# Kernel tuning notes

Measured on AMD Instinct MI355X. Metric: run time of the kernel, lower is better.

The kernel has to match this reference:

```python
import jax, jax.numpy as jnp
import numpy as np

DIM = 2048
HEAD = 256
SEQ = 4096

def setup_inputs() -> dict:
    key = jax.random.key(0)
    ks = jax.random.split(key, 7)
    s = 1.0 / np.sqrt(DIM)
    return {
        "marketStateBatch": jax.random.normal(ks[0], (SEQ, DIM), dtype=jnp.float32),
        "Wq": jax.random.uniform(ks[1], (HEAD, DIM), jnp.float32, -s, s),
        "bq": jax.random.uniform(ks[2], (HEAD,), jnp.float32, -s, s),
        "Wk": jax.random.uniform(ks[3], (HEAD, DIM), jnp.float32, -s, s),
        "bk": jax.random.uniform(ks[4], (HEAD,), jnp.float32, -s, s),
        "Wv": jax.random.uniform(ks[5], (HEAD, DIM), jnp.float32, -s, s),
        "bv": jax.random.uniform(ks[6], (HEAD,), jnp.float32, -s, s),
    }

def reference(marketStateBatch, Wq, bq, Wk, bk, Wv, bv):
    x = marketStateBatch  # [S, D]
    q = x @ Wq.T + bq     # [S, H]
    k = x @ Wk.T + bk     # [S, H]
    v = x @ Wv.T + bv     # [S, H]
    # NOTE: original scales by sqrt(dimensionSize), the INPUT dim, not head dim.
    scores = (q @ k.T) * (1.0 / np.sqrt(DIM))  # [S, S]
    S = x.shape[0]
    causal = jnp.tril(jnp.ones((S, S), dtype=bool))
    scores = jnp.where(causal, scores, -jnp.inf)
    attn = jax.nn.softmax(scores, axis=-1)
    # torch.nan_to_num(attn, 0.0): rows are never all -inf here (diag kept),
    # but replicate the op faithfully.
    attn = jnp.nan_to_num(attn, nan=0.0)
    return attn @ v  # [S, H]
```

## Files before the change

### kernel.cpp

```cpp
#include <hip/hip_runtime.h>
#include <stdint.h>

#define SEQ 4096
#define DIMK 2048
#define HD 256

typedef __attribute__((ext_vector_type(8))) short bf16x8;
typedef __attribute__((ext_vector_type(4))) short u16x4;
typedef __attribute__((ext_vector_type(4))) float f32x4;
typedef __attribute__((ext_vector_type(16))) float f32x16;
typedef unsigned short u16;
typedef unsigned int u32;

#define BAR() asm volatile("s_barrier" ::: "memory")
#define VMCNT(n) asm volatile("s_waitcnt vmcnt(" #n ")" ::: "memory")

__device__ __forceinline__ u16 f2bf(float f) {
    u32 u = __float_as_uint(f);
    u += 0x7FFFu + ((u >> 16) & 1u);
    return (u16)(u >> 16);
}

__device__ __forceinline__ float bf2f(u16 h) {
    u32 u = ((u32)h) << 16;
    return __uint_as_float(u);
}

__device__ __forceinline__ bf16x8 pack8(f32x4 a0, f32x4 a1) {
    bf16x8 v8;
    v8[0]=(short)f2bf(a0[0]); v8[1]=(short)f2bf(a0[1]);
    v8[2]=(short)f2bf(a0[2]); v8[3]=(short)f2bf(a0[3]);
    v8[4]=(short)f2bf(a1[0]); v8[5]=(short)f2bf(a1[1]);
    v8[6]=(short)f2bf(a1[2]); v8[7]=(short)f2bf(a1[3]);
    return v8;
}

__device__ __forceinline__ void gl16(const void* g, void* l) {
    __builtin_amdgcn_global_load_lds(
        (const __attribute__((address_space(1))) void*)g,
        (__attribute__((address_space(3))) void*)l, 16, 0, 0);
}

__device__ __forceinline__ u32 cvtpk(float lo, float hi) {
    u32 d;
    asm("v_cvt_pk_bf16_f32 %0, %1, %2" : "=v"(d) : "v"(lo), "v"(hi));
    return d;
}

__device__ __forceinline__ void plswap(u32& x, u32& y) {
#if __has_builtin(__builtin_amdgcn_permlane32_swap)
    typedef int i32x2 __attribute__((ext_vector_type(2)));
    i32x2 r = __builtin_amdgcn_permlane32_swap((int)x, (int)y, false, false);
    x = (u32)r[0]; y = (u32)r[1];
#else
    asm("v_permlane32_swap_b32 %0, %1" : "+v"(x), "+v"(y));
#endif
}

__global__ __launch_bounds__(256) void cvt_all2(
    const float* __restrict__ x, const float* __restrict__ Wq,
    const float* __restrict__ Wk, const float* __restrict__ Wv,
    u16* __restrict__ xb_sw, u16* __restrict__ wb_sw)
{
    const int y = blockIdx.y;
    int i = blockIdx.x * 256 + threadIdx.x;
    int stride = gridDim.x * 256;
    if (y == 0) {
        for (; i < SEQ*DIMK/8; i += stride) {
            int row = i >> 8, c8 = i & 255;
            f32x4 a0 = *(const f32x4*)(x + (size_t)row*DIMK + c8*8);
            f32x4 a1 = *(const f32x4*)(x + (size_t)row*DIMK + c8*8 + 4);
            int mt = row >> 6, rl = row & 63, kt = c8 >> 3, sl = c8 & 7;
            size_t dst = ((size_t)(mt*32 + kt))*4096 + rl*64 + ((sl ^ (rl&7))*8);
            *(bf16x8*)(xb_sw + dst) = pack8(a0, a1);
        }
    } else {
        const float* W = (y==1) ? Wq : (y==2) ? Wk : Wv;
        for (; i < HD*DIMK/8; i += stride) {
            int row = i >> 8, c8 = i & 255;
            f32x4 a0 = *(const f32x4*)(W + (size_t)row*DIMK + c8*8);
            f32x4 a1 = *(const f32x4*)(W + (size_t)row*DIMK + c8*8 + 4);
            int gr = (y-1)*256 + row;
            int nt = gr >> 7, rl = gr & 127, kt = c8 >> 3, sl = c8 & 7;
            size_t dst = ((size_t)(nt*32 + kt))*8192 + rl*64 + ((sl ^ (rl&7))*8);
            *(bf16x8*)(wb_sw + dst) = pack8(a0, a1);
        }
    }
}

__global__ __launch_bounds__(256) void qkv_gemm2(
    const u16* __restrict__ xb_sw, const u16* __restrict__ wb_sw,
    const float* __restrict__ bq, const float* __restrict__ bk,
    const float* __restrict__ bv,
    u16* __restrict__ qb, u16* __restrict__ kb_t, u16* __restrict__ vt_t)
{
    __shared__ char T[2][24576];

    const int tid = threadIdx.x;
    const int lane = tid & 63;
    const int w = tid >> 6;
    const int r = lane & 15, g = lane >> 4;
    const int wr = w >> 1, wc = w & 1;
    const int mt = blockIdx.x;
    const int y  = blockIdx.y;
    const int z  = y >> 1;
    const float* bias = (z==0) ? bq : (z==1) ? bk : bv;

    const u16* abase = xb_sw + (size_t)mt*32*4096;
    const u16* bbase = wb_sw + (size_t)y*32*8192;

    f32x4 zero = {0.f,0.f,0.f,0.f};
    f32x4 acc[2][4];
    #pragma unroll
    for (int m = 0; m < 2; ++m)
        #pragma unroll
        for (int n = 0; n < 4; ++n) acc[m][n] = zero;

    auto stage = [&](int b, int kt) {
        const u16* ag = abase + (size_t)kt*4096 + w*1024 + lane*8;
        const u16* bg = bbase + (size_t)kt*8192 + w*2048 + lane*8;
        char* al = T[b] + w*2048;
        char* bl = T[b] + 8192 + w*4096;
        gl16(ag,        al);
        gl16(ag + 512,  al + 1024);
        gl16(bg,        bl);
        gl16(bg + 512,  bl + 1024);
        gl16(bg + 1024, bl + 2048);
        gl16(bg + 1536, bl + 3072);
    };

    stage(0, 0);
    stage(1, 1);

    for (int kt = 0; kt < 32; ++kt) {
        if (kt < 31) { VMCNT(6); } else { VMCNT(0); }
        BAR();
        const char* A = T[kt & 1];
        const char* B = T[kt & 1] + 8192;
        #pragma unroll
        for (int kc = 0; kc < 2; ++kc) {
            bf16x8 af[2], bfr[4];
            #pragma unroll
            for (int m = 0; m < 2; ++m) {
                int arow = wr*32 + m*16 + r;
                af[m] = *(const bf16x8*)(A + arow*128 + (((kc*4+g) ^ (arow&7)) << 4));
            }
            #pragma unroll
            for (int n = 0; n < 4; ++n) {
                int brow = wc*64 + n*16 + r;
                bfr[n] = *(const bf16x8*)(B + brow*128 + (((kc*4+g) ^ (brow&7)) << 4));
            }
            #pragma unroll
            for (int m = 0; m < 2; ++m)
                #pragma unroll
                for (int n = 0; n < 4; ++n)
                    acc[m][n] = __builtin_amdgcn_mfma_f32_16x16x32_bf16(
                        af[m], bfr[n], acc[m][n], 0, 0, 0);
        }
        BAR();
        if (kt + 2 < 32) stage(kt & 1, kt + 2);
    }

    const int m0 = mt*64, n0 = y*128;
    const float qs = 0.03187936f;
    if (z == 0) {
        #pragma unroll
        for (int n = 0; n < 4; ++n) {
            int hc = (n0 + wc*64 + n*16 + r) & 255;
            float bcol = bias[hc];
            #pragma unroll
            for (int m = 0; m < 2; ++m) {
                int row0 = m0 + wr*32 + m*16 + g*4;
                #pragma unroll
                for (int j = 0; j < 4; ++j)
                    qb[(size_t)(row0+j)*HD + hc] = f2bf((acc[m][n][j] + bcol) * qs);
            }
        }
    } else if (z == 1) {
        #pragma unroll
        for (int n = 0; n < 4; ++n) {
            int hc = (n0 + wc*64 + n*16 + r) & 255;
            float bcol = bias[hc];
            #pragma unroll
            for (int m = 0; m < 2; ++m) {
                int row0 = m0 + wr*32 + m*16 + g*4;
                #pragma unroll
                for (int j = 0; j < 4; ++j) {
                    int rowj = row0 + j;
                    int t = rowj >> 5, rl = rowj & 31;
                    kb_t[(size_t)t*8192 + rl*256 + (((hc>>3) ^ (rl&7))*8) + (hc&7)]
                        = f2bf(acc[m][n][j] + bcol);
                }
            }
        }
    } else {
        #pragma unroll
        for (int n = 0; n < 4; ++n) {
            int hc = (n0 + wc*64 + n*16 + r) & 255;
            float bcol = bias[hc];
            #pragma unroll
            for (int m = 0; m < 2; ++m) {
                int kv0 = m0 + wr*32 + m*16 + g*4;
                int t = kv0 >> 5, kl = kv0 & 31;
                u16x4 pk;
                #pragma unroll
                for (int j = 0; j < 4; ++j) pk[j] = (short)f2bf(acc[m][n][j] + bcol);
                *(u16x4*)(vt_t + (size_t)t*8192 + hc*32 +
                          (((kl>>3) ^ (hc&3) ^ ((hc>>2)&3))*8) + (kl&7)) = pk;
            }
        }
    }
}

__global__ __launch_bounds__(256, 2) void attn_part6(
    const u16* __restrict__ qb, const u16* __restrict__ kb_t,
    const u16* __restrict__ vt_t,
    u16* __restrict__ po, float* __restrict__ pm, float* __restrict__ pl,
    int C)
{
    __shared__ char Kb[2][16384];
    __shared__ char Vb[2][16384];

    const int pid = blockIdx.x;
    int Q = 0, a0 = 0;
    for (int k = 0; k < 32; ++k) {
        int nsk = (4*k + 4 + C - 1) / C;
        if (pid < a0 + nsk) { Q = k; break; }
        a0 += nsk;
    }
    const int s  = pid - a0;
    const int nt = 4*Q + 4;
    const int t0 = s*C;
    const int t1 = min(t0 + C, nt);

    const int tid = threadIdx.x;
    const int L = tid & 63;
    const int w = tid >> 6;
    const int l31 = L & 31;
    const int h   = L >> 5;
    const int qg  = Q*128 + w*32 + l31;
    const int vsw = (l31 & 3) ^ ((l31 >> 2) & 3);
    const int kx  = l31 & 7;

    auto stage = [&](int t, int b) {
        const u16* kg = kb_t + (size_t)t*8192 + w*2048 + L*8;
        const u16* vg = vt_t + (size_t)t*8192 + w*2048 + L*8;
        char* kl = Kb[b] + w*4096;
        char* vl = Vb[b] + w*4096;
        #pragma unroll
        for (int i = 0; i < 4; ++i) gl16(kg + i*512, kl + i*1024);
        #pragma unroll
        for (int i = 0; i < 4; ++i) gl16(vg + i*512, vl + i*1024);
    };

    stage(t0, t0 & 1);
    if (t0 + 1 < t1) stage(t0 + 1, (t0 + 1) & 1);
    else             stage(t0,     (t0 + 1) & 1);

    bf16x8 qf[16];
    {
        const u16* qp = qb + (size_t)qg*HD + h*8;
        #pragma unroll
        for (int c = 0; c < 16; ++c) qf[c] = *(const bf16x8*)(qp + c*16);
    }

    f32x16 o[8];
    #pragma unroll
    for (int ht = 0; ht < 8; ++ht)
        #pragma unroll
        for (int e = 0; e < 16; ++e) o[ht][e] = 0.f;
    float mrun = -1e30f, lrun = 0.f;

    for (int t = t0; t < t1; ++t) {
        if (t + 1 < t1) { VMCNT(8); } else { VMCNT(0); }
        BAR();
        const char* K = Kb[t & 1];
        const char* V = Vb[t & 1];

        #define LDK(c) (*(const bf16x8*)(K + l31*512 + (((2*(c) + h) ^ kx) << 4)))
        f32x16 sv;
        #pragma unroll
        for (int e = 0; e < 16; ++e) sv[e] = 0.f;
        __builtin_amdgcn_s_setprio(1);
        {
            bf16x8 ka = LDK(0), kb_ = LDK(1), kc = LDK(2), kd = LDK(3);
            sv = __builtin_amdgcn_mfma_f32_32x32x16_bf16(ka,  qf[0],  sv, 0,0,0); ka  = LDK(4);
            sv = __builtin_amdgcn_mfma_f32_32x32x16_bf16(kb_, qf[1],  sv, 0,0,0); kb_ = LDK(5);
            sv = __builtin_amdgcn_mfma_f32_32x32x16_bf16(kc,  qf[2],  sv, 0,0,0); kc  = LDK(6);
            sv = __builtin_amdgcn_mfma_f32_32x32x16_bf16(kd,  qf[3],  sv, 0,0,0); kd  = LDK(7);
            sv = __builtin_amdgcn_mfma_f32_32x32x16_bf16(ka,  qf[4],  sv, 0,0,0); ka  = LDK(8);
            sv = __builtin_amdgcn_mfma_f32_32x32x16_bf16(kb_, qf[5],  sv, 0,0,0); kb_ = LDK(9);
            sv = __builtin_amdgcn_mfma_f32_32x32x16_bf16(kc,  qf[6],  sv, 0,0,0); kc  = LDK(10);
            sv = __builtin_amdgcn_mfma_f32_32x32x16_bf16(kd,  qf[7],  sv, 0,0,0); kd  = LDK(11);
            sv = __builtin_amdgcn_mfma_f32_32x32x16_bf16(ka,  qf[8],  sv, 0,0,0); ka  = LDK(12);
            sv = __builtin_amdgcn_mfma_f32_32x32x16_bf16(kb_, qf[9],  sv, 0,0,0); kb_ = LDK(13);
            sv = __builtin_amdgcn_mfma_f32_32x32x16_bf16(kc,  qf[10], sv, 0,0,0); kc  = LDK(14);
            sv = __builtin_amdgcn_mfma_f32_32x32x16_bf16(kd,  qf[11], sv, 0,0,0); kd  = LDK(15);
            sv = __builtin_amdgcn_mfma_f32_32x32x16_bf16(ka,  qf[12], sv, 0,0,0);
            sv = __builtin_amdgcn_mfma_f32_32x32x16_bf16(kb_, qf[13], sv, 0,0,0);
            sv = __builtin_amdgcn_mfma_f32_32x32x16_bf16(kc,  qf[14], sv, 0,0,0);
            sv = __builtin_amdgcn_mfma_f32_32x32x16_bf16(kd,  qf[15], sv, 0,0,0);
        }
        #undef LDK
        __builtin_amdgcn_s_setprio(0);

        if (t*32 + 31 > Q*128 + w*32) {
            #pragma unroll
            for (int e = 0; e < 16; ++e) {
                int kvr = (e & 3) + 8*(e >> 2) + 4*h;
                if (t*32 + kvr > qg) sv[e] = -__builtin_inff();
            }
        }

        float m0_ = fmaxf(fmaxf(sv[0],sv[1]),  fmaxf(sv[2],sv[3]));
        float m1_ = fmaxf(fmaxf(sv[4],sv[5]),  fmaxf(sv[6],sv[7]));
        float m2_ = fmaxf(fmaxf(sv[8],sv[9]),  fmaxf(sv[10],sv[11]));
        float m3_ = fmaxf(fmaxf(sv[12],sv[13]),fmaxf(sv[14],sv[15]));
        float mx = fmaxf(fmaxf(m0_,m1_), fmaxf(m2_,m3_));
        mx = fmaxf(mx, __shfl_xor(mx, 32));
        if (__any(mx > mrun + 8.0f)) {
            float mnew  = fmaxf(mrun, mx);
            float alpha = exp2f(mrun - mnew);
            lrun *= alpha;
            #pragma unroll
            for (int ht = 0; ht < 8; ++ht) o[ht] *= alpha;
            mrun = mnew;
        }
        #pragma unroll
        for (int e = 0; e < 16; ++e) sv[e] = exp2f(sv[e] - mrun);
        float r0 = ((sv[0]+sv[1])+(sv[2]+sv[3])) + ((sv[4]+sv[5])+(sv[6]+sv[7]));
        float r1 = ((sv[8]+sv[9])+(sv[10]+sv[11])) + ((sv[12]+sv[13])+(sv[14]+sv[15]));
        float rs = r0 + r1;
        rs += __shfl_xor(rs, 32);
        lrun += rs;

        union { u32 wd[4]; bf16x8 v8; } up0, up1;
        {
            u32 A = cvtpk(sv[0],  sv[1]),  B = cvtpk(sv[2],  sv[3]);
            u32 Cc= cvtpk(sv[4],  sv[5]),  D = cvtpk(sv[6],  sv[7]);
            plswap(A, Cc); plswap(B, D);
            up0.wd[0]=A; up0.wd[1]=B; up0.wd[2]=Cc; up0.wd[3]=D;
            u32 A1 = cvtpk(sv[8],  sv[9]),  B1 = cvtpk(sv[10], sv[11]);
            u32 C1 = cvtpk(sv[12], sv[13]), D1 = cvtpk(sv[14], sv[15]);
            plswap(A1, C1); plswap(B1, D1);
            up1.wd[0]=A1; up1.wd[1]=B1; up1.wd[2]=C1; up1.wd[3]=D1;
        }
        bf16x8 pa0 = up0.v8, pa1 = up1.v8;

        __builtin_amdgcn_s_setprio(1);
        #pragma unroll
        for (int ht = 0; ht < 8; ++ht) {
            const char* vrow = V + (ht*32 + l31)*64;
            bf16x8 vf0 = *(const bf16x8*)(vrow + (((h)     ^ vsw) << 4));
            bf16x8 vf1 = *(const bf16x8*)(vrow + (((2 + h) ^ vsw) << 4));
            o[ht] = __builtin_amdgcn_mfma_f32_32x32x16_bf16(vf0, pa0, o[ht], 0, 0, 0);
            o[ht] = __builtin_amdgcn_mfma_f32_32x32x16_bf16(vf1, pa1, o[ht], 0, 0, 0);
        }
        __builtin_amdgcn_s_setprio(0);

        BAR();
        stage(min(t + 2, t1 - 1), t & 1);
    }

    VMCNT(0);

    if (h == 0) {
        pm[(size_t)pid*128 + w*32 + l31] = mrun;
        pl[(size_t)pid*128 + w*32 + l31] = lrun;
    }
    u16* op = po + ((size_t)pid*128 + w*32 + l31) * 256;
    #pragma unroll
    for (int ht = 0; ht < 8; ++ht)
        #pragma unroll
        for (int j = 0; j < 8; ++j) {
            u32 pk = (u32)f2bf(o[ht][2*j]) | ((u32)f2bf(o[ht][2*j+1]) << 16);
            int hdb = ht*32 + (j & 1)*2 + (j >> 1)*8 + 4*h;
            *(u32*)(op + hdb) = pk;
        }
}

__global__ __launch_bounds__(256) void attn_combine5(
    const u16* __restrict__ po, const float* __restrict__ pm,
    const float* __restrict__ pl, float* __restrict__ out, int C)
{
    const int tid = threadIdx.x;
    const int row = blockIdx.x * 16 + (tid >> 4);
    const int cg  = tid & 15;
    const int Q   = row >> 7, rr = row & 127;
    const int nt  = 4*Q + 4;
    const int ns  = (nt + C - 1) / C;
    int pid0 = 0;
    for (int k = 0; k < Q; ++k) pid0 += (4*k + 4 + C - 1) / C;

    float M = -1e30f;
    for (int s = 0; s < ns; ++s)
        M = fmaxf(M, pm[(size_t)(pid0+s)*128 + rr]);

    float lt = 0.f;
    f32x4 acc[4];
    f32x4 zero = {0.f,0.f,0.f,0.f};
    #pragma unroll
    for (int v = 0; v < 4; ++v) acc[v] = zero;

    for (int s = 0; s < ns; ++s) {
        float ms  = pm[(size_t)(pid0+s)*128 + rr];
        float wgt = exp2f(ms - M);
        lt += wgt * pl[(size_t)(pid0+s)*128 + rr];
        const u16* p = po + ((size_t)(pid0+s)*128 + rr)*256 + cg*16;
        #pragma unroll
        for (int v = 0; v < 4; ++v) {
            u16x4 pv = *(const u16x4*)(p + v*4);
            #pragma unroll
            for (int e = 0; e < 4; ++e)
                acc[v][e] += wgt * bf2f((u16)pv[e]);
        }
    }
    float inv = 1.f / lt;
    f32x4* op = (f32x4*)(out + (size_t)row*256 + cg*16);
    #pragma unroll
    for (int v = 0; v < 4; ++v) op[v] = acc[v] * inv;
}

extern "C" void kernel_launch(void* const* d_in, const int* in_sizes, int n_in,
                              void* d_out, int out_size, void* d_ws, size_t ws_size,
                              hipStream_t stream) {
    const float* x  = (const float*)d_in[0];
    const float* Wq = (const float*)d_in[1];
    const float* bq = (const float*)d_in[2];
    const float* Wk = (const float*)d_in[3];
    const float* bk = (const float*)d_in[4];
    const float* Wv = (const float*)d_in[5];
    const float* bv = (const float*)d_in[6];
    float* out = (float*)d_out;

    const size_t xb_bytes  = (size_t)SEQ * DIMK * 2;
    const size_t wb_bytes  = (size_t)768 * DIMK * 2;
    const size_t qkv_bytes = (size_t)SEQ * HD * 2;
    const size_t base = xb_bytes + wb_bytes + 3*qkv_bytes;

    int C = 64;
    size_t npid = 0;
    const int cand[4] = {5, 8, 16, 64};
    for (int ci = 0; ci < 4; ++ci) {
        int c = cand[ci];
        size_t np = 0;
        for (int k = 0; k < 32; ++k) np += (size_t)(4*k + 4 + c - 1) / c;
        size_t need = base + np * ((size_t)128*256*2 + 2*128*4);
        if (need <= ws_size) { C = c; npid = np; break; }
        if (ci == 3) { C = c; npid = np; }
    }

    char* p = (char*)d_ws;
    u16* xb_sw = (u16*)p; p += xb_bytes;
    u16* wb_sw = (u16*)p; p += wb_bytes;
    u16* qbuf  = (u16*)p; p += qkv_bytes;
    u16* kb_t  = (u16*)p; p += qkv_bytes;
    u16* vt_t  = (u16*)p; p += qkv_bytes;
    u16* po    = (u16*)p; p += npid * 128 * 256 * 2;
    float* pm  = (float*)p; p += npid * 128 * 4;
    float* pl  = (float*)p; p += npid * 128 * 4;

    cvt_all2<<<dim3(512, 4), 256, 0, stream>>>(x, Wq, Wk, Wv, xb_sw, wb_sw);

    qkv_gemm2<<<dim3(SEQ/64, 6), 256, 0, stream>>>(
        xb_sw, wb_sw, bq, bk, bv, qbuf, kb_t, vt_t);

    attn_part6<<<(int)npid, 256, 0, stream>>>(
        qbuf, kb_t, vt_t, po, pm, pl, C);

    attn_combine5<<<SEQ/16, 256, 0, stream>>>(po, pm, pl, out, C);
}
```

Measured before the change: 79.17 us.

## Enlarge QKV GEMM tile to 128x128 using 32x32x16 MFMA

The QKV projection GEMM goes from 64x128 block tiles to 128x128, so each block stages twice as many A rows and the grid halves. Each wave now computes a 64x64 sub-tile with 32x32x16 bf16 MFMAs instead of 16x16x32, which means fewer LDS fragment loads per FLOP. The change also raises wave priority around the MFMA section and sets a two-blocks-per-CU launch bound. The costs are more LDS per block, more accumulator registers, and only 192 blocks in the grid, which may leave some CUs idle.

```diff
diff --git a/kernel.cpp b/kernel.cpp
--- a/kernel.cpp
+++ b/kernel.cpp
@@ -88,125 +88,118 @@
     }
 }
 
-__global__ __launch_bounds__(256) void qkv_gemm2(
+__global__ __launch_bounds__(256, 2) void qkv_gemm3(
     const u16* __restrict__ xb_sw, const u16* __restrict__ wb_sw,
     const float* __restrict__ bq, const float* __restrict__ bk,
     const float* __restrict__ bv,
     u16* __restrict__ qb, u16* __restrict__ kb_t, u16* __restrict__ vt_t)
 {
-    __shared__ char T[2][24576];
+    __shared__ char Ab[2][16384];
+    __shared__ char Bb[2][16384];
 
     const int tid = threadIdx.x;
-    const int lane = tid & 63;
+    const int L = tid & 63;
     const int w = tid >> 6;
-    const int r = lane & 15, g = lane >> 4;
+    const int l31 = L & 31, h = L >> 5;
     const int wr = w >> 1, wc = w & 1;
-    const int mt = blockIdx.x;
-    const int y  = blockIdx.y;
-    const int z  = y >> 1;
+    const int mt2 = blockIdx.x;
+    const int y   = blockIdx.y;
+    const int z   = y >> 1;
     const float* bias = (z==0) ? bq : (z==1) ? bk : bv;
 
-    const u16* abase = xb_sw + (size_t)mt*32*4096;
-    const u16* bbase = wb_sw + (size_t)y*32*8192;
-
-    f32x4 zero = {0.f,0.f,0.f,0.f};
-    f32x4 acc[2][4];
-    #pragma unroll
-    for (int m = 0; m < 2; ++m)
-        #pragma unroll
-        for (int n = 0; n < 4; ++n) acc[m][n] = zero;
-
-    auto stage = [&](int b, int kt) {
-        const u16* ag = abase + (size_t)kt*4096 + w*1024 + lane*8;
-        const u16* bg = bbase + (size_t)kt*8192 + w*2048 + lane*8;
-        char* al = T[b] + w*2048;
-        char* bl = T[b] + 8192 + w*4096;
-        gl16(ag,        al);
-        gl16(ag + 512,  al + 1024);
-        gl16(bg,        bl);
-        gl16(bg + 512,  bl + 1024);
-        gl16(bg + 1024, bl + 2048);
-        gl16(bg + 1536, bl + 3072);
+    const u16* a0 = xb_sw + ((size_t)((mt2*2 + (w>>1))*32))*4096 + (w&1)*2048 + L*8;
+    const u16* b0 = wb_sw + ((size_t)(y*32))*8192 + w*2048 + L*8;
+
+    auto stage = [&](int kt, int b) {
+        const u16* ag = a0 + (size_t)kt*4096;
+        const u16* bg = b0 + (size_t)kt*8192;
+        char* al = Ab[b] + w*4096;
+        char* bl = Bb[b] + w*4096;
+        #pragma unroll
+        for (int i = 0; i < 4; ++i) gl16(ag + i*512, al + i*1024);
+        #pragma unroll
+        for (int i = 0; i < 4; ++i) gl16(bg + i*512, bl + i*1024);
     };
 
     stage(0, 0);
     stage(1, 1);
 
+    f32x16 acc[2][2];
+    #pragma unroll
+    for (int m = 0; m < 2; ++m)
+        #pragma unroll
+        for (int n = 0; n < 2; ++n)
+            #pragma unroll
+            for (int e = 0; e < 16; ++e) acc[m][n][e] = 0.f;
+
     for (int kt = 0; kt < 32; ++kt) {
-        if (kt < 31) { VMCNT(6); } else { VMCNT(0); }
+        if (kt < 31) { VMCNT(8); } else { VMCNT(0); }
         BAR();
-        const char* A = T[kt & 1];
-        const char* B = T[kt & 1] + 8192;
-        #pragma unroll
-        for (int kc = 0; kc < 2; ++kc) {
-            bf16x8 af[2], bfr[4];
+        const char* A = Ab[kt & 1];
+        const char* B = Bb[kt & 1];
+        __builtin_amdgcn_s_setprio(1);
+        #pragma unroll
+        for (int c = 0; c < 4; ++c) {
+            const int sl = 2*c + h;
+            bf16x8 af[2], bfr[2];
             #pragma unroll
             for (int m = 0; m < 2; ++m) {
-                int arow = wr*32 + m*16 + r;
-                af[m] = *(const bf16x8*)(A + arow*128 + (((kc*4+g) ^ (arow&7)) << 4));
+                int row = wr*64 + m*32 + l31;
+                af[m] = *(const bf16x8*)(A + (row>>6)*8192 + (row&63)*128
+                                           + ((sl ^ (row&7)) << 4));
             }
             #pragma unroll
-            for (int n = 0; n < 4; ++n) {
-                int brow = wc*64 + n*16 + r;
-                bfr[n] = *(const bf16x8*)(B + brow*128 + (((kc*4+g) ^ (brow&7)) << 4));
+            for (int n = 0; n < 2; ++n) {
+                int brow = wc*64 + n*32 + l31;
+                bfr[n] = *(const bf16x8*)(B + brow*128 + ((sl ^ (brow&7)) << 4));
             }
             #pragma unroll
             for (int m = 0; m < 2; ++m)
                 #pragma unroll
-                for (int n = 0; n < 4; ++n)
-                    acc[m][n] = __builtin_amdgcn_mfma_f32_16x16x32_bf16(
+                for (int n = 0; n < 2; ++n)
+                    acc[m][n] = __builtin_amdgcn_mfma_f32_32x32x16_bf16(
                         af[m], bfr[n], acc[m][n], 0, 0, 0);
         }
+        __builtin_amdgcn_s_setprio(0);
         BAR();
-        if (kt + 2 < 32) stage(kt & 1, kt + 2);
-    }
-
-    const int m0 = mt*64, n0 = y*128;
+        if (kt + 2 < 32) stage(kt + 2, kt & 1);
+    }
+
+    const int m0 = mt2*128;
     const float qs = 0.03187936f;
-    if (z == 0) {
-        #pragma unroll
-        for (int n = 0; n < 4; ++n) {
-            int hc = (n0 + wc*64 + n*16 + r) & 255;
-            float bcol = bias[hc];
-            #pragma unroll
-            for (int m = 0; m < 2; ++m) {
-                int row0 = m0 + wr*32 + m*16 + g*4;
+    #pragma unroll
+    for (int n = 0; n < 2; ++n) {
+        const int hc = ((y&1)*128 + wc*64 + n*32 + l31) & 255;
+        const float bcol = bias[hc];
+        #pragma unroll
+        for (int m = 0; m < 2; ++m) {
+            const int rbase = m0 + wr*64 + m*32;
+            if (z == 0) {
                 #pragma unroll
-                for (int j = 0; j < 4; ++j)
-                    qb[(size_t)(row0+j)*HD + hc] = f2bf((acc[m][n][j] + bcol) * qs);
-            }
-        }
-    } else if (z == 1) {
-        #pragma unroll
-        for (int n = 0; n < 4; ++n) {
-            int hc = (n0 + wc*64 + n*16 + r) & 255;
-            float bcol = bias[hc];
-            #pragma unroll
-            for (int m = 0; m < 2; ++m) {
-                int row0 = m0 + wr*32 + m*16 + g*4;
+                for (int e = 0; e < 16; ++e) {
+                    int grow = rbase + (e&3) + 8*(e>>2) + 4*h;
+                    qb[(size_t)grow*HD + hc] = f2bf((acc[m][n][e] + bcol) * qs);
+                }
+            } else if (z == 1) {
                 #pragma unroll
-                for (int j = 0; j < 4; ++j) {
-                    int rowj = row0 + j;
-                    int t = rowj >> 5, rl = rowj & 31;
+                for (int e = 0; e < 16; ++e) {
+                    int grow = rbase + (e&3) + 8*(e>>2) + 4*h;
+                    int t = grow >> 5, rl = grow & 31;
                     kb_t[(size_t)t*8192 + rl*256 + (((hc>>3) ^ (rl&7))*8) + (hc&7)]
-                        = f2bf(acc[m][n][j] + bcol);
+                        = f2bf(acc[m][n][e] + bcol);
                 }
-            }
-        }
-    } else {
-        #pragma unroll
-        for (int n = 0; n < 4; ++n) {
-            int hc = (n0 + wc*64 + n*16 + r) & 255;
-            float bcol = bias[hc];
-            #pragma unroll
-            for (int m = 0; m < 2; ++m) {
-                int kv0 = m0 + wr*32 + m*16 + g*4;
-                int t = kv0 >> 5, kl = kv0 & 31;
-                u16x4 pk;
+            } else {
+                const int t = rbase >> 5;
                 #pragma unroll
-                for (int j = 0; j < 4; ++j) pk[j] = (short)f2bf(acc[m][n][j] + bcol);
-                *(u16x4*)(vt_t + (size_t)t*8192 + hc*32 +
-                          (((kl>>3) ^ (hc&3) ^ ((hc>>2)&3))*8) + (kl&7)) = pk;
+                for (int e4 = 0; e4 < 4; ++e4) {
+                    int kl0 = 8*e4 + 4*h;
+                    u16x4 pk;
+                    #pragma unroll
+                    for (int j = 0; j < 4; ++j)
+                        pk[j] = (short)f2bf(acc[m][n][e4*4 + j] + bcol);
+                    *(u16x4*)(vt_t + (size_t)t*8192 + hc*32 +
+                              ((e4 ^ (hc&3) ^ ((hc>>2)&3))*8) + (kl0&7)) = pk;
+                }
             }
         }
     }
@@ -462,7 +455,7 @@
 
     cvt_all2<<<dim3(512, 4), 256, 0, stream>>>(x, Wq, Wk, Wv, xb_sw, wb_sw);
 
-    qkv_gemm2<<<dim3(SEQ/64, 6), 256, 0, stream>>>(
+    qkv_gemm3<<<dim3(SEQ/128, 6), 256, 0, stream>>>(
         xb_sw, wb_sw, bq, bk, bv, qbuf, kb_t, vt_t);
 
     attn_part6<<<(int)npid, 256, 0, stream>>>(
```

Measured after the change: 93.06 us. 17.5% more time.
